# Kernel optimization log

Measured on AMD Instinct MI355X. Metric: run time of the kernel, lower is better.

Reference implementation:

```python
import jax, jax.numpy as jnp
import numpy as np
import math

B_SZ, T_LEN, DIM = 1, 1024, 1024
D_STATE, EXPAND, NUM_SCALES, CONV_K = 16, 2, 3, 4
D_INNER = EXPAND * DIM
EPS_LOG = 1e-38
LN_EPS = 1e-5


def _causal_dwconv(x, w, b):
    # x: (B,T,D), w: (D,1,K) depthwise, b: (D,). torch Conv1d(pad=K-1)[:, :, :T] == left-pad K-1 (causal).
    y = jax.lax.conv_general_dilated(
        jnp.transpose(x, (0, 2, 1)), w, window_strides=(1,),
        padding=[(CONV_K - 1, 0)], dimension_numbers=('NCH', 'OIH', 'NCH'),
        feature_group_count=w.shape[0])
    return jnp.transpose(y, (0, 2, 1)) + b


def _ssm_core(x, cw, cb, xw, dtw, dtb, Dp):
    # x: (B,T,d_inner)
    xc = jax.nn.silu(_causal_dwconv(x, cw, cb))
    proj = xc @ xw.T                               # (B,T,2*d_state)
    B_ssm, C_ssm = proj[..., :D_STATE], proj[..., D_STATE:]
    dt = jax.nn.softplus(B_ssm @ dtw.T + dtb)      # (B,T,d_inner)
    dt = jax.nn.softplus(dt)                       # selective_scan applies softplus a second time (faithful)
    A = -jnp.arange(1, D_STATE + 1, dtype=xc.dtype)  # (d_state,) == -A_init row, same for every d_inner channel
    dA = jnp.exp(dt[..., None] * A)                # (B,T,d_inner,d_state)
    dBx = dt[..., None] * B_ssm[:, :, None, :] * xc[..., None]
    log_dA = jnp.log(jnp.clip(dA, EPS_LOG))
    log_dBx = jnp.log(jnp.clip(dBx, EPS_LOG))
    # parallel_scan_cpu: h = exp(cumsum(log_dA) + logcumsumexp(log_dBx - cumsum(log_dA)))
    a_star = jnp.cumsum(log_dA, axis=1)
    h = jnp.exp(a_star + jax.lax.cumlogsumexp(log_dBx - a_star, axis=1))
    return jnp.einsum('bts,btds->btd', C_ssm, h) + Dp * xc


def _downsample(x, stride):
    if stride == 1:
        return x
    Bb, T, D = x.shape
    Tt = (T // stride) * stride
    return x[:, :Tt].reshape(Bb, Tt // stride, stride, D).mean(2)


def _upsample(x, T_out):
    # F.interpolate(mode='linear', align_corners=False)
    T_in = x.shape[1]
    if T_in == T_out:
        return x
    scale = T_in / T_out
    pos = jnp.clip((jnp.arange(T_out, dtype=jnp.float32) + 0.5) * scale - 0.5, 0.0, T_in - 1)
    lo = jnp.floor(pos).astype(jnp.int32)
    hi = jnp.minimum(lo + 1, T_in - 1)
    w = (pos - lo.astype(pos.dtype))[None, :, None]
    return x[:, lo] * (1.0 - w) + x[:, hi] * w


def _forward(x, in_proj_w, conv_w, conv_b, xproj_w, dtproj_w, dtproj_b,
             D_param, scale_weights, gate_w1, gate_w2, out_proj_w, ln_g, ln_b):
    residual = x
    xz = x @ in_proj_w.T                           # (B,T,2*d_inner)
    x_in, gate = xz[..., :D_INNER], xz[..., D_INNER:]
    outs = []
    for s in range(NUM_SCALES):
        x_s = _downsample(x_in, 2 ** s)
        y_s = _ssm_core(x_s, conv_w[s], conv_b[s], xproj_w[s], dtproj_w[s], dtproj_b[s], D_param[s])
        outs.append(_upsample(y_s, x.shape[1]))
    w = jax.nn.softmax(scale_weights)
    fused = sum(w[s] * outs[s] for s in range(NUM_SCALES))
    ctx = sum(outs) / NUM_SCALES
    gate_ctx = jax.nn.sigmoid(jax.nn.silu(ctx @ gate_w1.T) @ gate_w2.T)
    out = (fused * gate_ctx) * jax.nn.silu(gate)
    out = out @ out_proj_w.T
    y = out + residual
    mu = y.mean(-1, keepdims=True)
    var = ((y - mu) ** 2).mean(-1, keepdims=True)
    return (y - mu) / jnp.sqrt(var + LN_EPS) * ln_g + ln_b


def setup_inputs() -> dict:
    key = jax.random.key(0)
    ks = jax.random.split(key, 12)
    g = lambda k, shp, s: (jax.random.normal(k, shp, jnp.float32) * s)
    return {
        'x': g(ks[0], (B_SZ, T_LEN, DIM), 1.0),
        'in_proj_w': g(ks[1], (2 * D_INNER, DIM), DIM ** -0.5),
        'conv_w': g(ks[2], (NUM_SCALES, D_INNER, 1, CONV_K), CONV_K ** -0.5),
        'conv_b': g(ks[3], (NUM_SCALES, D_INNER), 0.02),
        'xproj_w': g(ks[4], (NUM_SCALES, 2 * D_STATE, D_INNER), D_INNER ** -0.5),
        'dtproj_w': g(ks[5], (NUM_SCALES, D_INNER, D_STATE), D_STATE ** -0.5),
        'dtproj_b': jax.random.uniform(ks[6], (NUM_SCALES, D_INNER), jnp.float32,
                                       math.log(0.001), math.log(0.1)),
        'D_param': jnp.ones((NUM_SCALES, D_INNER), jnp.float32),
        'scale_weights': jnp.ones((NUM_SCALES,), jnp.float32) / NUM_SCALES,
        'gate_w1': g(ks[7], (D_INNER // 2, D_INNER), D_INNER ** -0.5),
        'gate_w2': g(ks[8], (D_INNER, D_INNER // 2), (D_INNER // 2) ** -0.5),
        'out_proj_w': g(ks[9], (DIM, D_INNER), D_INNER ** -0.5),
        'ln_g': jnp.ones((DIM,), jnp.float32),
        'ln_b': jnp.zeros((DIM,), jnp.float32),
    }


def reference(x, in_proj_w, conv_w, conv_b, xproj_w, dtproj_w, dtproj_b,
              D_param, scale_weights, gate_w1, gate_w2, out_proj_w, ln_g, ln_b):
    return _forward(x, in_proj_w, conv_w, conv_b, xproj_w, dtproj_w, dtproj_b,
                    D_param, scale_weights, gate_w1, gate_w2, out_proj_w, ln_g, ln_b)
```

## Files before the change

### kernel.cpp

```cpp
#include <hip/hip_runtime.h>

typedef unsigned short u16;
typedef float floatx2 __attribute__((ext_vector_type(2)));
typedef float floatx4 __attribute__((ext_vector_type(4)));
typedef short shortx8 __attribute__((ext_vector_type(8)));

#define DIN 2048

__device__ __forceinline__ u16 f2bf(float f){
  unsigned u = __float_as_uint(f);
  u = (u + 0x7fffu + ((u>>16)&1u))>>16;
  return (u16)u;
}
__device__ __forceinline__ float sigf(float x){ return 1.f/(1.f+__expf(-x)); }
__device__ __forceinline__ float siluf(float x){ return x*sigf(x); }
__device__ __forceinline__ floatx2 max2(floatx2 a, floatx2 b){
  floatx2 r; r.x = fmaxf(a.x, b.x); r.y = fmaxf(a.y, b.y); return r;
}

#define OFF_WINP  0ull
#define OFF_WG1   8388608ull
#define OFF_WG2   12582912ull
#define OFF_WOP   16777216ull
#define OFF_XB    20971520ull
#define OFF_XIN   23068672ull
#define OFF_SGATE 31457280ull
#define OFF_X1    39845888ull
#define OFF_X2    44040192ull
#define OFF_XC0   46137344ull
#define OFF_XC1   54525952ull
#define OFF_XC2   58720256ull
#define OFF_FUSED 60817408ull
#define OFF_G3O   69206016ull
#define OFF_Y0    75497472ull
#define OFF_Y1    83886080ull
#define OFF_Y2    88080384ull
#define OFF_P0    90177536ull
#define OFF_P1    90308608ull
#define OFF_P2    90374144ull
#define OFF_PS    92274688ull
#define OFF_HINIT 121634816ull
#define OFF_CTXB  OFF_XC0
#define OFF_T1B   OFF_XC1
#define OFF_T1A0  OFF_XIN
#define OFF_T1A1  OFF_X1
#define OFF_YPA0  OFF_Y1
#define OFF_YPA1  (OFF_XC0 + 4194304ull)
#define OFF_DT0   OFF_FUSED
#define OFF_DT1   OFF_G3O
#define OFF_DT2   (OFF_G3O + 4194304ull)

__device__ __forceinline__ void gld_lds16(const void* g, void* l){
  __builtin_amdgcn_global_load_lds((const __attribute__((address_space(1))) unsigned*)g,
                                   (__attribute__((address_space(3))) unsigned*)l, 16, 0, 0);
}

__global__ __launch_bounds__(256) void cvt_kernel(
    const float* __restrict__ s0, u16* __restrict__ d0,
    const float* __restrict__ s1, u16* __restrict__ d1,
    const float* __restrict__ s2, u16* __restrict__ d2,
    const float* __restrict__ s3, u16* __restrict__ d3,
    const float* __restrict__ s4, u16* __restrict__ d4)
{
  int i = (blockIdx.x*256 + threadIdx.x)*4;
  const float* s; u16* d;
  if      (i <  4194304){ s=s0; d=d0; }
  else if (i <  6291456){ s=s1; d=d1; i -=  4194304; }
  else if (i <  8388608){ s=s2; d=d2; i -=  6291456; }
  else if (i < 10485760){ s=s3; d=d3; i -=  8388608; }
  else                  { s=s4; d=d4; i -= 10485760; }
  const float4 v = *(const float4*)(s + i);
  ushort4 o; o.x = f2bf(v.x); o.y = f2bf(v.y); o.z = f2bf(v.z); o.w = f2bf(v.w);
  *(ushort4*)(d + i) = o;
}

template<int MODE, int BM>
__global__ __launch_bounds__(256) void gemm_bt(
    const u16* __restrict__ A, const u16* __restrict__ B,
    int N, int K, int Ks,
    float* __restrict__ out_f, float* __restrict__ out_f2, u16* __restrict__ out_b,
    const float* __restrict__ ex0f, const float* __restrict__ ex1f,
    float* __restrict__ ex0, float* __restrict__ ex1)
{
  constexpr int NI = BM/32;
  constexpr int IP = BM/64;
  __shared__ u16 smA[2][BM*32];
  __shared__ u16 smB[2][BM*32];
  const int tid  = threadIdx.x;
  const int m0   = blockIdx.y * BM;
  const int n0   = blockIdx.x * BM;
  const int wv   = tid >> 6;
  const int lane = tid & 63;
  const int mw   = (wv >> 1) * (BM/2);
  const int nw   = (wv & 1) * (BM/2);
  const int quad = lane >> 4;
  const int l16  = lane & 15;
  const int srow = tid >> 2;
  const int scol = (tid & 3) * 8;

  floatx4 acc[NI][NI];
#pragma unroll
  for (int i=0;i<NI;i++)
#pragma unroll
    for (int j=0;j<NI;j++) acc[i][j] = (floatx4)0.f;

  const int kStart = blockIdx.z * Ks;
  const int kEnd   = kStart + Ks;

  auto stage = [&](int buf, int k0){
#pragma unroll
    for (int p=0;p<IP;p++){
      gld_lds16(A + (size_t)(m0 + p*64 + srow)*K + k0 + scol, &smA[buf][p*2048 + wv*512]);
      gld_lds16(B + (size_t)(n0 + p*64 + srow)*K + k0 + scol, &smB[buf][p*2048 + wv*512]);
    }
  };

  stage(0, kStart);
  int cur = 0;
  for (int k0 = kStart; k0 < kEnd; k0 += 32) {
    __syncthreads();
    if (k0 + 32 < kEnd) stage(cur^1, k0+32);
    shortx8 af[NI], bfr[NI];
#pragma unroll
    for (int i=0;i<NI;i++){
      af[i]  = *(const shortx8*)&smA[cur][(mw + i*16 + l16)*32 + quad*8];
      bfr[i] = *(const shortx8*)&smB[cur][(nw + i*16 + l16)*32 + quad*8];
    }
#pragma unroll
    for (int i=0;i<NI;i++)
#pragma unroll
      for (int j=0;j<NI;j++)
        acc[i][j] = __builtin_amdgcn_mfma_f32_16x16x32_bf16(af[i], bfr[j], acc[i][j], 0, 0, 0);
    cur ^= 1;
  }

#pragma unroll
  for (int i=0;i<NI;i++){
    const int mb = m0 + mw + i*16 + quad*4;
#pragma unroll
    for (int j=0;j<NI;j++){
      const int n = n0 + nw + j*16 + l16;
      const floatx4 v4 = acc[i][j];
      if (MODE == 0){
        if (n < 2048){
#pragma unroll
          for (int r=0;r<4;r++) out_f[(size_t)(mb+r)*2048 + n] = v4[r];
          ex0[(size_t)(mb>>1)*2048 + n]       = 0.5f*(v4[0]+v4[1]);
          ex0[(size_t)((mb>>1)+1)*2048 + n]   = 0.5f*(v4[2]+v4[3]);
          ex1[(size_t)(mb>>2)*2048 + n]       = 0.25f*(v4[0]+v4[1]+v4[2]+v4[3]);
        } else {
#pragma unroll
          for (int r=0;r<4;r++) out_f2[(size_t)(mb+r)*2048 + (n-2048)] = siluf(v4[r]);
        }
      } else if (MODE == 2){
#pragma unroll
        for (int r=0;r<4;r++){
          const size_t idx = (size_t)(mb+r)*N + n;
          out_b[idx] = f2bf(sigf(v4[r]) * ex0f[idx] * ex1f[idx]);
        }
      } else {
        float* dst = blockIdx.z ? out_f2 : out_f;
#pragma unroll
        for (int r=0;r<4;r++) dst[(size_t)(mb+r)*N + n] = v4[r];
      }
    }
  }
}

__global__ __launch_bounds__(256) void g2_epi(const float* __restrict__ a,
    const float* __restrict__ b, u16* __restrict__ o){
  const int i = (blockIdx.x*256 + threadIdx.x)*4;
  const float4 va = *(const float4*)(a+i);
  const float4 vb = *(const float4*)(b+i);
  ushort4 r;
  r.x = f2bf(siluf(va.x+vb.x)); r.y = f2bf(siluf(va.y+vb.y));
  r.z = f2bf(siluf(va.z+vb.z)); r.w = f2bf(siluf(va.w+vb.w));
  *(ushort4*)(o+i) = r;
}

__global__ __launch_bounds__(256) void conv_kernel(const float* __restrict__ xin,
    const float* __restrict__ x1, const float* __restrict__ x2,
    const float* __restrict__ cw, const float* __restrict__ cb,
    float* __restrict__ xc0, float* __restrict__ xc1, float* __restrict__ xc2){
  const int idx = blockIdx.x*256 + threadIdx.x;
  const float* xs; float* xc; int s, local;
  if (idx < 1024*DIN)              { s=0; local=idx;             xs=xin; xc=xc0; }
  else if (idx < (1024+512)*DIN)   { s=1; local=idx-1024*DIN;    xs=x1;  xc=xc1; }
  else                             { s=2; local=idx-1536*DIN;    xs=x2;  xc=xc2; }
  const int t = local >> 11, d = local & 2047;
  const float* w = cw + ((size_t)(s*DIN) + d)*4;
  float acc = cb[s*DIN + d];
#pragma unroll
  for (int j=0;j<4;j++){
    const int tt = t - 3 + j;
    if (tt >= 0) acc += w[j] * xs[(size_t)tt*DIN + d];
  }
  xc[local] = siluf(acc);
}

__global__ __launch_bounds__(256) void xproj_kernel(const float* __restrict__ xc0,
    const float* __restrict__ xc1, const float* __restrict__ xc2,
    const float* __restrict__ xw,
    float* __restrict__ p0, float* __restrict__ p1, float* __restrict__ p2){
  __shared__ float srow[DIN];
  const int b = blockIdx.x;
  const float* xc; float* proj; int s, t;
  if (b < 1024)      { s=0; t=b;       xc=xc0; proj=p0; }
  else if (b < 1536) { s=1; t=b-1024;  xc=xc1; proj=p1; }
  else               { s=2; t=b-1536;  xc=xc2; proj=p2; }
  const float* xr = xc + (size_t)t*DIN;
  const int tid = threadIdx.x;
#pragma unroll
  for (int q=0;q<2;q++){
    const int k = (q*256 + tid)*4;
    *(float4*)&srow[k] = *(const float4*)&xr[k];
  }
  __syncthreads();
  const int i = tid >> 3;
  const int j = tid & 7;
  const float* w = xw + ((size_t)s*32 + i)*DIN;
  float acc = 0.f;
#pragma unroll 8
  for (int c=0;c<256;c++){
    const int k = j + 8*c;
    acc += srow[k]*w[k];
  }
  acc += __shfl_xor(acc,1); acc += __shfl_xor(acc,2); acc += __shfl_xor(acc,4);
  if (j == 0) proj[t*32 + i] = acc;
}

__global__ __launch_bounds__(128) void scan_p1(
    const float* __restrict__ xc0, const float* __restrict__ xc1, const float* __restrict__ xc2,
    const float* __restrict__ p0,  const float* __restrict__ p1,  const float* __restrict__ p2,
    const float* __restrict__ dtw, const float* __restrict__ dtb,
    float* __restrict__ dt0, float* __restrict__ dt1, float* __restrict__ dt2,
    float2* __restrict__ PS)
{
  __shared__ float sproj[16*32];
  int b = blockIdx.x;
  const float *xc, *proj; float* dto; int base, s;
  if (b < 1024)      { xc=xc0; proj=p0; dto=dt0; base=0;  s=0; }
  else if (b < 1536) { b-=1024; xc=xc1; proj=p1; dto=dt1; base=64; s=1; }
  else               { b-=1536; xc=xc2; proj=p2; dto=dt2; base=96; s=2; }
  const int chunk = b >> 4;
  const int tid   = threadIdx.x;
  const int d     = (b & 15)*128 + tid;
  const int t0    = chunk*16;
  {
    const int k = tid*4;
    *(float4*)&sproj[k] = *(const float4*)&proj[t0*32 + k];
  }
  __syncthreads();

  floatx2 w2[8];
  const floatx2* wr = (const floatx2*)(dtw + ((size_t)(s*DIN) + d)*16);
#pragma unroll
  for (int k=0;k<8;k++) w2[k] = wr[k];
  const float bias = dtb[s*DIN + d];
  const floatx2 eps2 = {1e-38f, 1e-38f};

  floatx2 H2[8];
#pragma unroll
  for (int k=0;k<8;k++) H2[k] = (floatx2)0.f;
  float S = 0.f;
  const float* xcp = xc + (size_t)t0*DIN + d;
  float* dtp = dto + (size_t)t0*DIN + d;
  for (int tt=0; tt<16; tt++){
    const float xcv = xcp[(size_t)tt*DIN];
    const floatx2* Bp2 = (const floatx2*)&sproj[tt*32];
    floatx2 zz = (floatx2)0.f;
#pragma unroll
    for (int k=0;k<8;k++) zz += Bp2[k]*w2[k];
    float z = fminf(zz.x + zz.y + bias, 60.f);
    const float E     = __expf(z);
    const float denom = 2.f + E;
    const float e     = __builtin_amdgcn_rcpf(denom);
    const float dtv   = __logf(denom);
    dtp[(size_t)tt*DIN] = dtv;
    S += dtv;
    const floatx2 c2  = {dtv*xcv, dtv*xcv};
    const floatx2 es  = {e*e, e*e};
    floatx2 ep2 = {e, e*e};
#pragma unroll
    for (int k=0;k<8;k++){
      const floatx2 dA  = max2(ep2, eps2);
      const floatx2 dBx = max2(c2*Bp2[k], eps2);
      H2[k] = dA*H2[k] + dBx;
      ep2 *= es;
    }
  }
  const float q = __expf(-S);
  const floatx2 qs = {q*q, q*q};
  floatx2 qp2 = {q, q*q};
  float2* o = PS + ((size_t)(base+chunk)*2048 + d)*16;
#pragma unroll
  for (int k=0;k<8;k++){
    float2 v0; v0.x = qp2.x; v0.y = H2[k].x; o[2*k]   = v0;
    float2 v1; v1.x = qp2.y; v1.y = H2[k].y; o[2*k+1] = v1;
    qp2 *= qs;
  }
}

__global__ __launch_bounds__(256) void scan_combine(const float2* __restrict__ PS,
                                                    float* __restrict__ Hinit){
  int id = blockIdx.x*256 + threadIdx.x;
  int base, C;
  if (id < 32768)      { base=0;  C=64; }
  else if (id < 65536) { id-=32768; base=64; C=32; }
  else                 { id-=65536; base=96; C=16; }
  const size_t off = (size_t)base*32768 + id;
  const float2* ps = PS + off;
  float* hi = Hinit + off;
  float H = 0.f;
  for (int c=0;c<C;c++){
    hi[(size_t)c*32768] = H;
    const float2 v = ps[(size_t)c*32768];
    H = v.x*H + v.y;
  }
}

__global__ __launch_bounds__(128) void scan_p2(
    const float* __restrict__ xc0, const float* __restrict__ xc1, const float* __restrict__ xc2,
    const float* __restrict__ p0,  const float* __restrict__ p1,  const float* __restrict__ p2,
    const float* __restrict__ dt0, const float* __restrict__ dt1, const float* __restrict__ dt2,
    const float* __restrict__ Hinit, const float* __restrict__ Dp_all,
    float* __restrict__ y0, float* __restrict__ y1, float* __restrict__ y2)
{
  __shared__ float sproj[16*32];
  int b = blockIdx.x;
  const float *xc, *proj, *dti; float* y; int base, s;
  if (b < 1024)      { xc=xc0; proj=p0; dti=dt0; y=y0; base=0;  s=0; }
  else if (b < 1536) { b-=1024; xc=xc1; proj=p1; dti=dt1; y=y1; base=64; s=1; }
  else               { b-=1536; xc=xc2; proj=p2; dti=dt2; y=y2; base=96; s=2; }
  const int chunk = b >> 4;
  const int tid   = threadIdx.x;
  const int d     = (b & 15)*128 + tid;
  const int t0    = chunk*16;
  {
    const int k = tid*4;
    *(float4*)&sproj[k] = *(const float4*)&proj[t0*32 + k];
  }
  __syncthreads();

  floatx2 H2[8];
  const floatx2* hi = (const floatx2*)(Hinit + ((size_t)(base+chunk)*2048 + d)*16);
#pragma unroll
  for (int k=0;k<8;k++) H2[k] = hi[k];
  const float Dv = Dp_all[s*DIN + d];
  const floatx2 eps2 = {1e-38f, 1e-38f};
  const float* xcp = xc + (size_t)t0*DIN + d;
  const float* dtp = dti + (size_t)t0*DIN + d;
  float* yp = y + (size_t)t0*DIN + d;
  for (int tt=0; tt<16; tt++){
    const float xcv = xcp[(size_t)tt*DIN];
    const float dtv = dtp[(size_t)tt*DIN];
    const floatx2* Bp2 = (const floatx2*)&sproj[tt*32];
    const float e = __expf(-dtv);
    const floatx2 c2 = {dtv*xcv, dtv*xcv};
    const floatx2 es = {e*e, e*e};
    floatx2 ep2 = {e, e*e};
    floatx2 pacc2 = (floatx2)0.f;
#pragma unroll
    for (int k=0;k<8;k++){
      const floatx2 dA  = max2(ep2, eps2);
      const floatx2 dBx = max2(c2*Bp2[k], eps2);
      H2[k] = dA*H2[k] + dBx;
      pacc2 += Bp2[8+k]*H2[k];
      ep2 *= es;
    }
    yp[(size_t)tt*DIN] = pacc2.x + pacc2.y + Dv*xcv;
  }
}

__device__ __forceinline__ float ups_read(const float* __restrict__ ys, int Tin, int t, int d){
  const float scale = (float)Tin * (1.f/1024.f);
  float pos = ((float)t + 0.5f)*scale - 0.5f;
  pos = fminf(fmaxf(pos, 0.f), (float)(Tin-1));
  const int lo = (int)floorf(pos);
  const float w = pos - (float)lo;
  const int hi = min(lo+1, Tin-1);
  return ys[(size_t)lo*DIN + d]*(1.f-w) + ys[(size_t)hi*DIN + d]*w;
}

__global__ __launch_bounds__(256) void fuse_kernel(const float* __restrict__ y0,
    const float* __restrict__ y1, const float* __restrict__ y2,
    const float* __restrict__ sw, u16* __restrict__ ctxb, float* __restrict__ fused){
  const int idx = blockIdx.x*256 + threadIdx.x;
  const int t = idx >> 11, d = idx & 2047;
  const float w0r = sw[0], w1r = sw[1], w2r = sw[2];
  const float mx = fmaxf(w0r, fmaxf(w1r, w2r));
  float e0 = __expf(w0r-mx), e1 = __expf(w1r-mx), e2 = __expf(w2r-mx);
  const float inv = 1.f/(e0+e1+e2);
  e0 *= inv; e1 *= inv; e2 *= inv;
  const float o0 = y0[idx];
  const float o1 = ups_read(y1, 512, t, d);
  const float o2 = ups_read(y2, 256, t, d);
  fused[idx] = e0*o0 + e1*o1 + e2*o2;
  ctxb[idx]  = f2bf((o0+o1+o2)*(1.f/3.f));
}

__global__ __launch_bounds__(256) void ln_kernel(const float* __restrict__ ya,
    const float* __restrict__ yb, const float* __restrict__ xr,
    const float* __restrict__ g, const float* __restrict__ b, float* __restrict__ out){
  __shared__ float red[4];
  const int t = blockIdx.x;
  const size_t ro = (size_t)t*1024;
  float v[4];
  float s = 0.f;
#pragma unroll
  for (int i=0;i<4;i++){
    const int c = threadIdx.x + i*256;
    v[i] = ya[ro+c] + yb[ro+c] + xr[ro+c];
    s += v[i];
  }
  s += __shfl_xor(s,1); s += __shfl_xor(s,2); s += __shfl_xor(s,4);
  s += __shfl_xor(s,8); s += __shfl_xor(s,16); s += __shfl_xor(s,32);
  if ((threadIdx.x & 63) == 0) red[threadIdx.x>>6] = s;
  __syncthreads();
  const float mu = (red[0]+red[1]+red[2]+red[3]) * (1.f/1024.f);
  __syncthreads();
  float q = 0.f;
#pragma unroll
  for (int i=0;i<4;i++){ const float dd = v[i]-mu; q += dd*dd; }
  q += __shfl_xor(q,1); q += __shfl_xor(q,2); q += __shfl_xor(q,4);
  q += __shfl_xor(q,8); q += __shfl_xor(q,16); q += __shfl_xor(q,32);
  if ((threadIdx.x & 63) == 0) red[threadIdx.x>>6] = q;
  __syncthreads();
  const float rstd = rsqrtf((red[0]+red[1]+red[2]+red[3]) * (1.f/1024.f) + 1e-5f);
#pragma unroll
  for (int i=0;i<4;i++){
    const int c = threadIdx.x + i*256;
    out[ro + c] = (v[i]-mu)*rstd*g[c] + b[c];
  }
}

extern "C" void kernel_launch(void* const* d_in, const int* in_sizes, int n_in,
                              void* d_out, int out_size, void* d_ws, size_t ws_size,
                              hipStream_t stream) {
  const float* x     = (const float*)d_in[0];
  const float* inpw  = (const float*)d_in[1];
  const float* convw = (const float*)d_in[2];
  const float* convb = (const float*)d_in[3];
  const float* xpw   = (const float*)d_in[4];
  const float* dtw   = (const float*)d_in[5];
  const float* dtb   = (const float*)d_in[6];
  const float* Dp    = (const float*)d_in[7];
  const float* sw    = (const float*)d_in[8];
  const float* gw1   = (const float*)d_in[9];
  const float* gw2   = (const float*)d_in[10];
  const float* opw   = (const float*)d_in[11];
  const float* lng   = (const float*)d_in[12];
  const float* lnb   = (const float*)d_in[13];
  float* out = (float*)d_out;

  char* ws = (char*)d_ws;
  u16*    wInp  = (u16*)   (ws + OFF_WINP);
  u16*    wG1   = (u16*)   (ws + OFF_WG1);
  u16*    wG2   = (u16*)   (ws + OFF_WG2);
  u16*    wOp   = (u16*)   (ws + OFF_WOP);
  u16*    xb    = (u16*)   (ws + OFF_XB);
  float*  xin   = (float*) (ws + OFF_XIN);
  float*  sgate = (float*) (ws + OFF_SGATE);
  float*  x1    = (float*) (ws + OFF_X1);
  float*  x2    = (float*) (ws + OFF_X2);
  float*  xc0   = (float*) (ws + OFF_XC0);
  float*  xc1   = (float*) (ws + OFF_XC1);
  float*  xc2   = (float*) (ws + OFF_XC2);
  float*  dt0   = (float*) (ws + OFF_DT0);
  float*  dt1   = (float*) (ws + OFF_DT1);
  float*  dt2   = (float*) (ws + OFF_DT2);
  float*  y0    = (float*) (ws + OFF_Y0);
  float*  y1    = (float*) (ws + OFF_Y1);
  float*  y2    = (float*) (ws + OFF_Y2);
  float*  p0    = (float*) (ws + OFF_P0);
  float*  p1    = (float*) (ws + OFF_P1);
  float*  p2    = (float*) (ws + OFF_P2);
  float2* PS    = (float2*)(ws + OFF_PS);
  float*  Hinit = (float*) (ws + OFF_HINIT);
  u16*    ctxb  = (u16*)   (ws + OFF_CTXB);
  u16*    t1b   = (u16*)   (ws + OFF_T1B);
  float*  fused = (float*) (ws + OFF_FUSED);
  u16*    g3o   = (u16*)   (ws + OFF_G3O);
  float*  t1a0  = (float*) (ws + OFF_T1A0);
  float*  t1a1  = (float*) (ws + OFF_T1A1);
  float*  ypa0  = (float*) (ws + OFF_YPA0);
  float*  ypa1  = (float*) (ws + OFF_YPA1);

  cvt_kernel<<<11264, 256, 0, stream>>>(inpw, wInp, gw1, wG1, gw2, wG2, opw, wOp, x, xb);
  gemm_bt<0,64><<<dim3(64, 16, 1), 256, 0, stream>>>(xb, wInp, 4096, 1024, 1024,
                                                     xin, sgate, nullptr, nullptr, nullptr, x1, x2);
  conv_kernel<<<(1792*DIN)/256, 256, 0, stream>>>(xin, x1, x2, convw, convb, xc0, xc1, xc2);
  xproj_kernel<<<1792, 256, 0, stream>>>(xc0, xc1, xc2, xpw, p0, p1, p2);
  scan_p1<<<1792, 128, 0, stream>>>(xc0, xc1, xc2, p0, p1, p2, dtw, dtb,
                                    dt0, dt1, dt2, PS);
  scan_combine<<<384, 256, 0, stream>>>(PS, Hinit);
  scan_p2<<<1792, 128, 0, stream>>>(xc0, xc1, xc2, p0, p1, p2, dt0, dt1, dt2,
                                    Hinit, Dp, y0, y1, y2);
  fuse_kernel<<<(1024*DIN)/256, 256, 0, stream>>>(y0, y1, y2, sw, ctxb, fused);
  gemm_bt<4,64><<<dim3(16, 16, 2), 256, 0, stream>>>(ctxb, wG1, 1024, 2048, 1024,
                                                     t1a0, t1a1, nullptr, nullptr, nullptr, nullptr, nullptr);
  g2_epi<<<1024, 256, 0, stream>>>(t1a0, t1a1, t1b);
  gemm_bt<2,64><<<dim3(32, 16, 1), 256, 0, stream>>>(t1b, wG2, 2048, 1024, 1024,
                                                     nullptr, nullptr, g3o, fused, sgate, nullptr, nullptr);
  gemm_bt<4,64><<<dim3(16, 16, 2), 256, 0, stream>>>(g3o, wOp, 1024, 2048, 1024,
                                                     ypa0, ypa1, nullptr, nullptr, nullptr, nullptr, nullptr);
  ln_kernel<<<1024, 256, 0, stream>>>(ypa0, ypa1, x, lng, lnb, out);
}
```

Before: 299.5 us.

## Fuse causal conv with x-projection and store gate intermediates in bf16

```diff
diff --git a/kernel.cpp b/kernel.cpp
--- a/kernel.cpp
+++ b/kernel.cpp
@@ -12,6 +12,7 @@
   u = (u + 0x7fffu + ((u>>16)&1u))>>16;
   return (u16)u;
 }
+__device__ __forceinline__ float bf2f(u16 h){ return __uint_as_float(((unsigned)h)<<16); }
 __device__ __forceinline__ float sigf(float x){ return 1.f/(1.f+__expf(-x)); }
 __device__ __forceinline__ float siluf(float x){ return x*sigf(x); }
 __device__ __forceinline__ floatx2 max2(floatx2 a, floatx2 b){
@@ -46,7 +47,7 @@
 #define OFF_T1A1  OFF_X1
 #define OFF_YPA0  OFF_Y1
 #define OFF_YPA1  (OFF_XC0 + 4194304ull)
-#define OFF_DT0   OFF_FUSED
+#define OFF_DT0   60817408ull
 #define OFF_DT1   OFF_G3O
 #define OFF_DT2   (OFF_G3O + 4194304ull)
 
@@ -79,7 +80,7 @@
     const u16* __restrict__ A, const u16* __restrict__ B,
     int N, int K, int Ks,
     float* __restrict__ out_f, float* __restrict__ out_f2, u16* __restrict__ out_b,
-    const float* __restrict__ ex0f, const float* __restrict__ ex1f,
+    const u16* __restrict__ aux0b, const u16* __restrict__ aux1b,
     float* __restrict__ ex0, float* __restrict__ ex1)
 {
   constexpr int NI = BM/32;
@@ -150,13 +151,13 @@
           ex1[(size_t)(mb>>2)*2048 + n]       = 0.25f*(v4[0]+v4[1]+v4[2]+v4[3]);
         } else {
 #pragma unroll
-          for (int r=0;r<4;r++) out_f2[(size_t)(mb+r)*2048 + (n-2048)] = siluf(v4[r]);
+          for (int r=0;r<4;r++) out_b[(size_t)(mb+r)*2048 + (n-2048)] = f2bf(siluf(v4[r]));
         }
       } else if (MODE == 2){
 #pragma unroll
         for (int r=0;r<4;r++){
           const size_t idx = (size_t)(mb+r)*N + n;
-          out_b[idx] = f2bf(sigf(v4[r]) * ex0f[idx] * ex1f[idx]);
+          out_b[idx] = f2bf(sigf(v4[r]) * bf2f(aux0b[idx & 2097151]) * bf2f(aux1b[idx]));
         }
       } else {
         float* dst = blockIdx.z ? out_f2 : out_f;
@@ -178,55 +179,67 @@
   *(ushort4*)(o+i) = r;
 }
 
-__global__ __launch_bounds__(256) void conv_kernel(const float* __restrict__ xin,
-    const float* __restrict__ x1, const float* __restrict__ x2,
+__global__ __launch_bounds__(256) void convxproj_kernel(
+    const float* __restrict__ xin, const float* __restrict__ x1, const float* __restrict__ x2,
     const float* __restrict__ cw, const float* __restrict__ cb,
-    float* __restrict__ xc0, float* __restrict__ xc1, float* __restrict__ xc2){
-  const int idx = blockIdx.x*256 + threadIdx.x;
-  const float* xs; float* xc; int s, local;
-  if (idx < 1024*DIN)              { s=0; local=idx;             xs=xin; xc=xc0; }
-  else if (idx < (1024+512)*DIN)   { s=1; local=idx-1024*DIN;    xs=x1;  xc=xc1; }
-  else                             { s=2; local=idx-1536*DIN;    xs=x2;  xc=xc2; }
-  const int t = local >> 11, d = local & 2047;
-  const float* w = cw + ((size_t)(s*DIN) + d)*4;
-  float acc = cb[s*DIN + d];
+    const float* __restrict__ xw,
+    float* __restrict__ xc0, float* __restrict__ xc1, float* __restrict__ xc2,
+    float* __restrict__ p0, float* __restrict__ p1, float* __restrict__ p2)
+{
+  __shared__ float srow[DIN];
+  const int b = blockIdx.x;
+  const float* xs; float* xc; float* proj; int s, t;
+  if (b < 1024)      { s=0; t=b;       xs=xin; xc=xc0; proj=p0; }
+  else if (b < 1536) { s=1; t=b-1024;  xs=x1;  xc=xc1; proj=p1; }
+  else               { s=2; t=b-1536;  xs=x2;  xc=xc2; proj=p2; }
+  const int tid = threadIdx.x;
+  const int d0  = tid*8;
+
+  float acc[8];
+  {
+    const float4 b0 = *(const float4*)&cb[s*DIN + d0];
+    const float4 b1 = *(const float4*)&cb[s*DIN + d0 + 4];
+    acc[0]=b0.x; acc[1]=b0.y; acc[2]=b0.z; acc[3]=b0.w;
+    acc[4]=b1.x; acc[5]=b1.y; acc[6]=b1.z; acc[7]=b1.w;
+  }
+  float w[8][4];
+#pragma unroll
+  for (int q=0;q<8;q++){
+    const float4 wv = *(const float4*)&cw[((size_t)(s*DIN) + d0 + q)*4];
+    w[q][0]=wv.x; w[q][1]=wv.y; w[q][2]=wv.z; w[q][3]=wv.w;
+  }
 #pragma unroll
   for (int j=0;j<4;j++){
     const int tt = t - 3 + j;
-    if (tt >= 0) acc += w[j] * xs[(size_t)tt*DIN + d];
-  }
-  xc[local] = siluf(acc);
-}
-
-__global__ __launch_bounds__(256) void xproj_kernel(const float* __restrict__ xc0,
-    const float* __restrict__ xc1, const float* __restrict__ xc2,
-    const float* __restrict__ xw,
-    float* __restrict__ p0, float* __restrict__ p1, float* __restrict__ p2){
-  __shared__ float srow[DIN];
-  const int b = blockIdx.x;
-  const float* xc; float* proj; int s, t;
-  if (b < 1024)      { s=0; t=b;       xc=xc0; proj=p0; }
-  else if (b < 1536) { s=1; t=b-1024;  xc=xc1; proj=p1; }
-  else               { s=2; t=b-1536;  xc=xc2; proj=p2; }
-  const float* xr = xc + (size_t)t*DIN;
-  const int tid = threadIdx.x;
-#pragma unroll
-  for (int q=0;q<2;q++){
-    const int k = (q*256 + tid)*4;
-    *(float4*)&srow[k] = *(const float4*)&xr[k];
-  }
+    if (tt >= 0){
+      const float4 v0 = *(const float4*)&xs[(size_t)tt*DIN + d0];
+      const float4 v1 = *(const float4*)&xs[(size_t)tt*DIN + d0 + 4];
+      acc[0] += w[0][j]*v0.x; acc[1] += w[1][j]*v0.y;
+      acc[2] += w[2][j]*v0.z; acc[3] += w[3][j]*v0.w;
+      acc[4] += w[4][j]*v1.x; acc[5] += w[5][j]*v1.y;
+      acc[6] += w[6][j]*v1.z; acc[7] += w[7][j]*v1.w;
+    }
+  }
+  float4 r0, r1;
+  r0.x = siluf(acc[0]); r0.y = siluf(acc[1]); r0.z = siluf(acc[2]); r0.w = siluf(acc[3]);
+  r1.x = siluf(acc[4]); r1.y = siluf(acc[5]); r1.z = siluf(acc[6]); r1.w = siluf(acc[7]);
+  *(float4*)&xc[(size_t)t*DIN + d0]     = r0;
+  *(float4*)&xc[(size_t)t*DIN + d0 + 4] = r1;
+  *(float4*)&srow[d0]     = r0;
+  *(float4*)&srow[d0 + 4] = r1;
   __syncthreads();
+
   const int i = tid >> 3;
   const int j = tid & 7;
-  const float* w = xw + ((size_t)s*32 + i)*DIN;
-  float acc = 0.f;
+  const float* wp = xw + ((size_t)s*32 + i)*DIN;
+  float pa = 0.f;
 #pragma unroll 8
   for (int c=0;c<256;c++){
     const int k = j + 8*c;
-    acc += srow[k]*w[k];
-  }
-  acc += __shfl_xor(acc,1); acc += __shfl_xor(acc,2); acc += __shfl_xor(acc,4);
-  if (j == 0) proj[t*32 + i] = acc;
+    pa += srow[k]*wp[k];
+  }
+  pa += __shfl_xor(pa,1); pa += __shfl_xor(pa,2); pa += __shfl_xor(pa,4);
+  if (j == 0) proj[t*32 + i] = pa;
 }
 
 __global__ __launch_bounds__(128) void scan_p1(
@@ -384,7 +397,7 @@
 
 __global__ __launch_bounds__(256) void fuse_kernel(const float* __restrict__ y0,
     const float* __restrict__ y1, const float* __restrict__ y2,
-    const float* __restrict__ sw, u16* __restrict__ ctxb, float* __restrict__ fused){
+    const float* __restrict__ sw, u16* __restrict__ ctxb, u16* __restrict__ fusedb){
   const int idx = blockIdx.x*256 + threadIdx.x;
   const int t = idx >> 11, d = idx & 2047;
   const float w0r = sw[0], w1r = sw[1], w2r = sw[2];
@@ -395,8 +408,8 @@
   const float o0 = y0[idx];
   const float o1 = ups_read(y1, 512, t, d);
   const float o2 = ups_read(y2, 256, t, d);
-  fused[idx] = e0*o0 + e1*o1 + e2*o2;
-  ctxb[idx]  = f2bf((o0+o1+o2)*(1.f/3.f));
+  fusedb[idx] = f2bf(e0*o0 + e1*o1 + e2*o2);
+  ctxb[idx]   = f2bf((o0+o1+o2)*(1.f/3.f));
 }
 
 __global__ __launch_bounds__(256) void ln_kernel(const float* __restrict__ ya,
@@ -454,54 +467,54 @@
   float* out = (float*)d_out;
 
   char* ws = (char*)d_ws;
-  u16*    wInp  = (u16*)   (ws + OFF_WINP);
-  u16*    wG1   = (u16*)   (ws + OFF_WG1);
-  u16*    wG2   = (u16*)   (ws + OFF_WG2);
-  u16*    wOp   = (u16*)   (ws + OFF_WOP);
-  u16*    xb    = (u16*)   (ws + OFF_XB);
-  float*  xin   = (float*) (ws + OFF_XIN);
-  float*  sgate = (float*) (ws + OFF_SGATE);
-  float*  x1    = (float*) (ws + OFF_X1);
-  float*  x2    = (float*) (ws + OFF_X2);
-  float*  xc0   = (float*) (ws + OFF_XC0);
-  float*  xc1   = (float*) (ws + OFF_XC1);
-  float*  xc2   = (float*) (ws + OFF_XC2);
-  float*  dt0   = (float*) (ws + OFF_DT0);
-  float*  dt1   = (float*) (ws + OFF_DT1);
-  float*  dt2   = (float*) (ws + OFF_DT2);
-  float*  y0    = (float*) (ws + OFF_Y0);
-  float*  y1    = (float*) (ws + OFF_Y1);
-  float*  y2    = (float*) (ws + OFF_Y2);
-  float*  p0    = (float*) (ws + OFF_P0);
-  float*  p1    = (float*) (ws + OFF_P1);
-  float*  p2    = (float*) (ws + OFF_P2);
-  float2* PS    = (float2*)(ws + OFF_PS);
-  float*  Hinit = (float*) (ws + OFF_HINIT);
-  u16*    ctxb  = (u16*)   (ws + OFF_CTXB);
-  u16*    t1b   = (u16*)   (ws + OFF_T1B);
-  float*  fused = (float*) (ws + OFF_FUSED);
-  u16*    g3o   = (u16*)   (ws + OFF_G3O);
-  float*  t1a0  = (float*) (ws + OFF_T1A0);
-  float*  t1a1  = (float*) (ws + OFF_T1A1);
-  float*  ypa0  = (float*) (ws + OFF_YPA0);
-  float*  ypa1  = (float*) (ws + OFF_YPA1);
+  u16*    wInp   = (u16*)   (ws + OFF_WINP);
+  u16*    wG1    = (u16*)   (ws + OFF_WG1);
+  u16*    wG2    = (u16*)   (ws + OFF_WG2);
+  u16*    wOp    = (u16*)   (ws + OFF_WOP);
+  u16*    xb     = (u16*)   (ws + OFF_XB);
+  float*  xin    = (float*) (ws + OFF_XIN);
+  u16*    sgateb = (u16*)   (ws + OFF_SGATE);
+  float*  x1     = (float*) (ws + OFF_X1);
+  float*  x2     = (float*) (ws + OFF_X2);
+  float*  xc0    = (float*) (ws + OFF_XC0);
+  float*  xc1    = (float*) (ws + OFF_XC1);
+  float*  xc2    = (float*) (ws + OFF_XC2);
+  float*  dt0    = (float*) (ws + OFF_DT0);
+  float*  dt1    = (float*) (ws + OFF_DT1);
+  float*  dt2    = (float*) (ws + OFF_DT2);
+  float*  y0     = (float*) (ws + OFF_Y0);
+  float*  y1     = (float*) (ws + OFF_Y1);
+  float*  y2     = (float*) (ws + OFF_Y2);
+  float*  p0     = (float*) (ws + OFF_P0);
+  float*  p1     = (float*) (ws + OFF_P1);
+  float*  p2     = (float*) (ws + OFF_P2);
+  float2* PS     = (float2*)(ws + OFF_PS);
+  float*  Hinit  = (float*) (ws + OFF_HINIT);
+  u16*    ctxb   = (u16*)   (ws + OFF_CTXB);
+  u16*    t1b    = (u16*)   (ws + OFF_T1B);
+  u16*    fusedb = (u16*)   (ws + OFF_FUSED);
+  u16*    g3o    = (u16*)   (ws + OFF_G3O);
+  float*  t1a0   = (float*) (ws + OFF_T1A0);
+  float*  t1a1   = (float*) (ws + OFF_T1A1);
+  float*  ypa0   = (float*) (ws + OFF_YPA0);
+  float*  ypa1   = (float*) (ws + OFF_YPA1);
 
   cvt_kernel<<<11264, 256, 0, stream>>>(inpw, wInp, gw1, wG1, gw2, wG2, opw, wOp, x, xb);
   gemm_bt<0,64><<<dim3(64, 16, 1), 256, 0, stream>>>(xb, wInp, 4096, 1024, 1024,
-                                                     xin, sgate, nullptr, nullptr, nullptr, x1, x2);
-  conv_kernel<<<(1792*DIN)/256, 256, 0, stream>>>(xin, x1, x2, convw, convb, xc0, xc1, xc2);
-  xproj_kernel<<<1792, 256, 0, stream>>>(xc0, xc1, xc2, xpw, p0, p1, p2);
+                                                     xin, nullptr, sgateb, nullptr, nullptr, x1, x2);
+  convxproj_kernel<<<1792, 256, 0, stream>>>(xin, x1, x2, convw, convb, xpw,
+                                             xc0, xc1, xc2, p0, p1, p2);
   scan_p1<<<1792, 128, 0, stream>>>(xc0, xc1, xc2, p0, p1, p2, dtw, dtb,
                                     dt0, dt1, dt2, PS);
   scan_combine<<<384, 256, 0, stream>>>(PS, Hinit);
   scan_p2<<<1792, 128, 0, stream>>>(xc0, xc1, xc2, p0, p1, p2, dt0, dt1, dt2,
                                     Hinit, Dp, y0, y1, y2);
-  fuse_kernel<<<(1024*DIN)/256, 256, 0, stream>>>(y0, y1, y2, sw, ctxb, fused);
+  fuse_kernel<<<(1024*DIN)/256, 256, 0, stream>>>(y0, y1, y2, sw, ctxb, fusedb);
   gemm_bt<4,64><<<dim3(16, 16, 2), 256, 0, stream>>>(ctxb, wG1, 1024, 2048, 1024,
                                                      t1a0, t1a1, nullptr, nullptr, nullptr, nullptr, nullptr);
   g2_epi<<<1024, 256, 0, stream>>>(t1a0, t1a1, t1b);
   gemm_bt<2,64><<<dim3(32, 16, 1), 256, 0, stream>>>(t1b, wG2, 2048, 1024, 1024,
-                                                     nullptr, nullptr, g3o, fused, sgate, nullptr, nullptr);
+                                                     nullptr, nullptr, g3o, fusedb, sgateb, nullptr, nullptr);
   gemm_bt<4,64><<<dim3(16, 16, 2), 256, 0, stream>>>(g3o, wOp, 1024, 2048, 1024,
                                                      ypa0, ypa1, nullptr, nullptr, nullptr, nullptr, nullptr);
   ln_kernel<<<1024, 256, 0, stream>>>(ypa0, ypa1, x, lng, lnb, out);
```

New measurement: 299.7 us. About the same (+0.0%).
